# Kernel tuning notes

Measured on AMD Instinct MI355X. Metric: run time of the kernel, lower is better.

## Reference

```python
import jax, jax.numpy as jnp
import numpy as np
from jax import lax

# sRGB linear -> LMS matrix (Oklab M1)
M1 = jnp.array([[0.4122214708, 0.5363325363, 0.0514459929],
                [0.2119034982, 0.6806995451, 0.1073969566],
                [0.0883024619, 0.2817188376, 0.6299787005]], dtype=jnp.float32)
# LMS^(1/3) -> Oklab matrix (Oklab M2)
M2 = jnp.array([[0.2104542553, 0.7936177850, -0.0040720468],
                [1.9779984951, -2.4285922050, 0.4505937099],
                [0.0259040371, 0.7827717662, -0.8086757660]], dtype=jnp.float32)
_SX = jnp.array([[-1., 0., 1.], [-2., 0., 2.], [-1., 0., 1.]], dtype=jnp.float32)
_SY = jnp.array([[-1., -2., -1.], [0., 0., 0.], [1., 2., 1.]], dtype=jnp.float32)
SOBEL = jnp.stack([_SX, _SY])[:, None]  # (2,1,3,3) cross-correlation kernels

CLOSING_KERNEL = 11
CLOSING_PAD = CLOSING_KERNEL // 2
EDGE_THRESHOLD = 0.5
POST_DILATION = 2
EPS = 0.01


def _srgb_to_linear(srgb):
    srgb = jnp.clip(srgb, 0.0, 1.0)
    return jnp.where(srgb <= 0.04045, srgb / 12.92, ((srgb + 0.055) / 1.055) ** 2.4)


def _rgb_to_oklab(rgb):  # [B,3,H,W] -> [B,3,H,W]
    linear = _srgb_to_linear(rgb)
    lms = jnp.einsum('oc,bchw->bohw', M1, linear)
    lms = jnp.clip(lms, 1e-10, None) ** (1.0 / 3.0)
    return jnp.einsum('oc,bchw->bohw', M2, lms)


def _max_pool(x, k, p):  # torch max_pool2d pads with -inf implicitly
    return lax.reduce_window(x, -jnp.inf, lax.max, (1, 1, k, k), (1, 1, 1, 1),
                             [(0, 0), (0, 0), (p, p), (p, p)])


def _min_pool(x, k, p):  # -max_pool(-x): padding becomes +inf
    return lax.reduce_window(x, jnp.inf, lax.min, (1, 1, k, k), (1, 1, 1, 1),
                             [(0, 0), (0, 0), (p, p), (p, p)])


def _omni_edge(img):  # [B,C,H,W] -> [B,1,H,W]
    B, C, H, W = img.shape
    flat = img.reshape(B * C, 1, H, W)
    g = lax.conv_general_dilated(flat, SOBEL, (1, 1), [(1, 1), (1, 1)])  # [B*C,2,H,W]
    grad = (jnp.abs(g[:, 0]) + jnp.abs(g[:, 1])).reshape(B, C, H, W)
    return jnp.max(grad, axis=1, keepdims=True)


def _crevice_mask(target):
    edge_soft = jnp.clip(_omni_edge(target) / EDGE_THRESHOLD, 0.0, 1.0)
    dilated = _max_pool(edge_soft, CLOSING_KERNEL, CLOSING_PAD)
    closed = _min_pool(dilated, CLOSING_KERNEL, CLOSING_PAD)
    mask = jax.nn.relu(closed - edge_soft)
    if POST_DILATION > 0:
        dk = 2 * POST_DILATION + 1
        mask = _max_pool(mask, dk, POST_DILATION)
    return mask


def setup_inputs() -> dict:
    key = jax.random.key(0)
    k1, k2 = jax.random.split(key)
    shape = (8, 3, 1024, 1024)
    pred = jax.random.uniform(k1, shape, dtype=jnp.float32)
    target = jax.random.uniform(k2, shape, dtype=jnp.float32)
    return {"pred": pred, "target": target}


def reference(pred, target):
    crevice_mask = _crevice_mask(target)
    mask_sum = jnp.maximum(crevice_mask.sum(), 1.0)
    pred_lab = _rgb_to_oklab(pred)
    target_lab = _rgb_to_oklab(target)
    p_a, p_b = pred_lab[:, 1:2], pred_lab[:, 2:3]
    t_a, t_b = target_lab[:, 1:2], target_lab[:, 2:3]
    C_pred = jnp.sqrt(p_a ** 2 + p_b ** 2 + 1e-12)
    C_gt = jnp.sqrt(t_a ** 2 + t_b ** 2 + 1e-12)
    chroma_loss = (jnp.abs(C_pred - C_gt) * crevice_mask).sum() / mask_sum
    dot_ab = p_a * t_a + p_b * t_b
    cos_hue_diff = jnp.clip(dot_ab / (C_pred * C_gt + 1e-12), -1.0, 1.0)
    hue_loss = (jnp.clip(C_gt, EPS, None) * (1.0 - cos_hue_diff) * crevice_mask).sum() / mask_sum
    return chroma_loss + 2.0 * hue_loss
```

## Files before the change

kernel.cpp:

```cpp
#include <hip/hip_runtime.h>
#include <math.h>

#define K1_NR 16
#define SROWS 64
#define PCH   16
#define QCAP  1024


__device__ __forceinline__ float srgb_to_linear(float x) {
    x = fminf(fmaxf(x, 0.0f), 1.0f);
    return (x <= 0.04045f) ? x * (1.0f / 12.92f)
                           : powf((x + 0.055f) * (1.0f / 1.055f), 2.4f);
}

__device__ __forceinline__ void oklab_ab(float r, float g, float b,
                                         float& A, float& Bc) {
    r = srgb_to_linear(r);
    g = srgb_to_linear(g);
    b = srgb_to_linear(b);
    float l = 0.4122214708f * r + 0.5363325363f * g + 0.0514459929f * b;
    float m = 0.2119034982f * r + 0.6806995451f * g + 0.1073969566f * b;
    float s = 0.0883024619f * r + 0.2817188376f * g + 0.6299787005f * b;
    l = cbrtf(fmaxf(l, 1e-10f));
    m = cbrtf(fmaxf(m, 1e-10f));
    s = cbrtf(fmaxf(s, 1e-10f));
    A  = 1.9779984951f * l - 2.428592205f * m + 0.4505937099f * s;
    Bc = 0.0259040371f * l + 0.7827717662f * m - 0.808675766f  * s;
}

__device__ __forceinline__ void color_terms(const float* __restrict__ pred,
                                            const float* __restrict__ target,
                                            size_t off, size_t HWp, float m,
                                            float& sc, float& sh) {
    float pa, pb, ta, tb;
    oklab_ab(pred[off], pred[off + HWp], pred[off + 2 * HWp], pa, pb);
    oklab_ab(target[off], target[off + HWp], target[off + 2 * HWp], ta, tb);
    float Cp = sqrtf(pa * pa + pb * pb + 1e-12f);
    float Cg = sqrtf(ta * ta + tb * tb + 1e-12f);
    sc += fabsf(Cp - Cg) * m;
    float cosd = (pa * ta + pb * tb) / (Cp * Cg + 1e-12f);
    cosd = fminf(fmaxf(cosd, -1.0f), 1.0f);
    sh += fmaxf(Cg, 0.01f) * (1.0f - cosd) * m;
}


__global__ __launch_bounds__(256) void k1_edge(const float* __restrict__ target,
                                               float* __restrict__ edge,
                                               int H, int W) {
    int strips = H / K1_NR;
    int b   = blockIdx.x / strips;
    int ysi = blockIdx.x % strips;
    int lane = threadIdx.x & 63, q = threadIdx.x >> 6;
    int C0 = q << 8;
    int col0 = C0 + (lane << 2);
    int y0 = ysi * K1_NR;
    size_t HW = (size_t)H * W;
    const float* tb = target + (size_t)b * 3 * HW;
    float* ep = edge + (size_t)b * HW;

    int hcol = (lane == 0) ? (C0 - 1) : (C0 + 256);
    bool hen = (lane == 0 || lane == 63) && (hcol >= 0) && (hcol < W);
    int lm = (lane + 63) & 63, lp = (lane + 1) & 63;

    float4 pr[3], cu[3], nx[3];
    float hpr[3], hcu[3], hnx[3];
#pragma unroll
    for (int c = 0; c < 3; ++c) {
        const float* p = tb + (size_t)c * HW;
        if (y0 > 0) {
            pr[c]  = *(const float4*)(p + (size_t)(y0 - 1) * W + col0);
            hpr[c] = hen ? p[(size_t)(y0 - 1) * W + hcol] : 0.f;
        } else {
            pr[c] = make_float4(0.f, 0.f, 0.f, 0.f);
            hpr[c] = 0.f;
        }
        cu[c]  = *(const float4*)(p + (size_t)y0 * W + col0);
        hcu[c] = hen ? p[(size_t)y0 * W + hcol] : 0.f;
    }

#pragma unroll 2
    for (int y = y0; y < y0 + K1_NR; ++y) {
        bool okn = (y + 1 < H);
#pragma unroll
        for (int c = 0; c < 3; ++c) {
            const float* p = tb + (size_t)c * HW + (size_t)(y + 1) * W;
            nx[c]  = okn ? *(const float4*)(p + col0)
                         : make_float4(0.f, 0.f, 0.f, 0.f);
            hnx[c] = (okn && hen) ? p[hcol] : 0.f;
        }
        float4 g = make_float4(0.f, 0.f, 0.f, 0.f);
#pragma unroll
        for (int c = 0; c < 3; ++c) {
            float4 u, v;
            u.x = fmaf(2.f, cu[c].x, pr[c].x) + nx[c].x;
            u.y = fmaf(2.f, cu[c].y, pr[c].y) + nx[c].y;
            u.z = fmaf(2.f, cu[c].z, pr[c].z) + nx[c].z;
            u.w = fmaf(2.f, cu[c].w, pr[c].w) + nx[c].w;
            v.x = nx[c].x - pr[c].x;
            v.y = nx[c].y - pr[c].y;
            v.z = nx[c].z - pr[c].z;
            v.w = nx[c].w - pr[c].w;
            float hu = fmaf(2.f, hcu[c], hpr[c]) + hnx[c];
            float hv = hnx[c] - hpr[c];
            float um1 = __shfl(u.w, lm); if (lane == 0)  um1 = hu;
            float up4 = __shfl(u.x, lp); if (lane == 63) up4 = hu;
            float vm1 = __shfl(v.w, lm); if (lane == 0)  vm1 = hv;
            float vp4 = __shfl(v.x, lp); if (lane == 63) vp4 = hv;
            float4 gx, gy;
            gx.x = u.y - um1; gx.y = u.z - u.x; gx.z = u.w - u.y; gx.w = up4 - u.z;
            gy.x = fmaf(2.f, v.x, vm1) + v.y;
            gy.y = fmaf(2.f, v.y, v.x) + v.z;
            gy.z = fmaf(2.f, v.z, v.y) + v.w;
            gy.w = fmaf(2.f, v.w, v.z) + vp4;
            g.x = fmaxf(g.x, fabsf(gx.x) + fabsf(gy.x));
            g.y = fmaxf(g.y, fabsf(gx.y) + fabsf(gy.y));
            g.z = fmaxf(g.z, fabsf(gx.z) + fabsf(gy.z));
            g.w = fmaxf(g.w, fabsf(gx.w) + fabsf(gy.w));
        }
        float4 e;
        e.x = fminf(2.f * g.x, 1.f);
        e.y = fminf(2.f * g.y, 1.f);
        e.z = fminf(2.f * g.z, 1.f);
        e.w = fminf(2.f * g.w, 1.f);
        *(float4*)(ep + (size_t)y * W + col0) = e;
#pragma unroll
        for (int c = 0; c < 3; ++c) {
            pr[c] = cu[c]; cu[c] = nx[c];
            hpr[c] = hcu[c]; hcu[c] = hnx[c];
        }
    }
}


template <int R, bool ISMAX, bool SUB_EDGE>
__global__ __launch_bounds__(256) void pool_kernel(const float* __restrict__ in,
                                                   const float* __restrict__ edge,
                                                   float* __restrict__ out,
                                                   int H, int W) {
    const int OUTW = 256 - 2 * R;
    __shared__ float s_v[PCH][256];
    int cb = (W + OUTW - 1) / OUTW;
    int rs = H / SROWS;
    int blk = blockIdx.x;
    int b   = blk / (cb * rs);
    int t   = blk % (cb * rs);
    int bxi = t / rs, ysi = t % rs;
    int tid = threadIdx.x;
    int col = bxi * OUTW - R + tid;
    int cc  = min(max(col, 0), W - 1);
    size_t base = (size_t)b * H * W;
    const float* colp = in + base + cc;
    int ys = ysi * SROWS;
    bool writer = (tid >= R) && (tid < OUTW + R) && (col < W);

    for (int ph = 0; ph < SROWS / PCH; ++ph) {
        int y0 = ys + ph * PCH;
        float w[PCH + 2 * R];
#pragma unroll
        for (int k = 0; k < PCH + 2 * R; ++k) {
            int r = min(max(y0 - R + k, 0), H - 1);
            w[k] = colp[(size_t)r * W];
        }
        float v[PCH];
#pragma unroll
        for (int k = 0; k < PCH; ++k) {
            float m = w[k];
#pragma unroll
            for (int d = 1; d <= 2 * R; ++d)
                m = ISMAX ? fmaxf(m, w[k + d]) : fminf(m, w[k + d]);
            v[k] = m;
        }
        __syncthreads();
#pragma unroll
        for (int k = 0; k < PCH; ++k) s_v[k][tid] = v[k];
        __syncthreads();
        if (writer) {
#pragma unroll
            for (int k = 0; k < PCH; ++k) {
                float m = s_v[k][tid - R];
#pragma unroll
                for (int d = 1; d <= 2 * R; ++d)
                    m = ISMAX ? fmaxf(m, s_v[k][tid - R + d])
                              : fminf(m, s_v[k][tid - R + d]);
                size_t gi = base + (size_t)(y0 + k) * W + col;
                out[gi] = SUB_EDGE ? fmaxf(m - edge[gi], 0.f) : m;
            }
        }
    }
}


__global__ __launch_bounds__(256) void k4_loss(const float* __restrict__ pred,
                                               const float* __restrict__ target,
                                               const float* __restrict__ mask0,
                                               float* __restrict__ partials,
                                               int H, int W, int nb) {
    const int R = 2, OUTW = 256 - 2 * R;
    __shared__ float s_v[PCH][256];
    __shared__ int   q_pos[QCAP];
    __shared__ float q_m[QCAP];
    __shared__ int   cnt;
    __shared__ float s_red[3][4];

    int cb = (W + OUTW - 1) / OUTW;
    int rs = H / SROWS;
    int blk = blockIdx.x;
    int b   = blk / (cb * rs);
    int t   = blk % (cb * rs);
    int bxi = t / rs, ysi = t % rs;
    int tid = threadIdx.x;
    int col = bxi * OUTW - R + tid;
    int cc  = min(max(col, 0), W - 1);
    size_t HWp  = (size_t)H * W;
    size_t base = (size_t)b * HWp;
    size_t cbase = (size_t)b * 3 * HWp;
    const float* colp = mask0 + base + cc;
    int ys = ysi * SROWS;
    bool writer = (tid >= R) && (tid < OUTW + R) && (col < W);

    float sm = 0.f, sc = 0.f, sh = 0.f;

    for (int ph = 0; ph < SROWS / PCH; ++ph) {
        int y0 = ys + ph * PCH;
        float w[PCH + 2 * R];
#pragma unroll
        for (int k = 0; k < PCH + 2 * R; ++k) {
            int r = min(max(y0 - R + k, 0), H - 1);
            w[k] = colp[(size_t)r * W];
        }
        float v[PCH];
#pragma unroll
        for (int k = 0; k < PCH; ++k) {
            float m = w[k];
#pragma unroll
            for (int d = 1; d <= 2 * R; ++d) m = fmaxf(m, w[k + d]);
            v[k] = m;
        }
        __syncthreads();
#pragma unroll
        for (int k = 0; k < PCH; ++k) s_v[k][tid] = v[k];
        if (tid == 0) cnt = 0;
        __syncthreads();
        if (writer) {
#pragma unroll
            for (int k = 0; k < PCH; ++k) {
                float m = s_v[k][tid - R];
#pragma unroll
                for (int d = 1; d <= 2 * R; ++d)
                    m = fmaxf(m, s_v[k][tid - R + d]);
                sm += m;
                if (m > 0.f) {
                    int pos = atomicAdd(&cnt, 1);
                    if (pos < QCAP) {
                        q_pos[pos] = ((y0 + k) << 16) | col;
                        q_m[pos] = m;
                    } else {
                        color_terms(pred, target,
                                    cbase + (size_t)(y0 + k) * W + col,
                                    HWp, m, sc, sh);
                    }
                }
            }
        }
        __syncthreads();
        int n = min(cnt, QCAP);
        for (int i = tid; i < n; i += 256) {
            int pk = q_pos[i];
            color_terms(pred, target,
                        cbase + (size_t)(pk >> 16) * W + (pk & 0xffff),
                        HWp, q_m[i], sc, sh);
        }
    }

#pragma unroll
    for (int off = 32; off > 0; off >>= 1) {
        sm += __shfl_down(sm, off);
        sc += __shfl_down(sc, off);
        sh += __shfl_down(sh, off);
    }
    int lane = tid & 63, wav = tid >> 6;
    __syncthreads();
    if (lane == 0) { s_red[0][wav] = sm; s_red[1][wav] = sc; s_red[2][wav] = sh; }
    __syncthreads();
    if (tid == 0) {
        float tm = 0, tc = 0, th = 0;
        for (int i = 0; i < 4; ++i) {
            tm += s_red[0][i]; tc += s_red[1][i]; th += s_red[2][i];
        }
        partials[blk]          = tm;
        partials[nb + blk]     = tc;
        partials[2 * nb + blk] = th;
    }
}

__global__ void finalize_kernel(const float* __restrict__ partials, int nb,
                                float* __restrict__ out) {
    double sm = 0.0, sc = 0.0, sh = 0.0;
    for (int i = threadIdx.x; i < nb; i += blockDim.x) {
        sm += (double)partials[i];
        sc += (double)partials[nb + i];
        sh += (double)partials[2 * nb + i];
    }
    __shared__ double red[3][256];
    red[0][threadIdx.x] = sm;
    red[1][threadIdx.x] = sc;
    red[2][threadIdx.x] = sh;
    __syncthreads();
    for (int s = blockDim.x / 2; s > 0; s >>= 1) {
        if ((int)threadIdx.x < s) {
            red[0][threadIdx.x] += red[0][threadIdx.x + s];
            red[1][threadIdx.x] += red[1][threadIdx.x + s];
            red[2][threadIdx.x] += red[2][threadIdx.x + s];
        }
        __syncthreads();
    }
    if (threadIdx.x == 0) {
        double ms = fmax(red[0][0], 1.0);
        out[0] = (float)(red[1][0] / ms + 2.0 * red[2][0] / ms);
    }
}


extern "C" void kernel_launch(void* const* d_in, const int* in_sizes, int n_in,
                              void* d_out, int out_size, void* d_ws, size_t ws_size,
                              hipStream_t stream) {
    const float* pred   = (const float*)d_in[0];
    const float* target = (const float*)d_in[1];
    float* out = (float*)d_out;

    const int H = 1024, W = 1024;
    int Bn = in_sizes[0] / (3 * H * W);
    size_t plane = (size_t)Bn * H * W * sizeof(float);

    char* ws = (char*)d_ws;
    float* planeA = (float*)ws;
    float* planeB = (float*)(ws + plane);
    float* partials = (float*)(ws + 2 * plane);

    int g1 = Bn * (H / K1_NR);
    int rs = H / SROWS;
    int cbP = (W + 245) / 246;
    int cb4 = (W + 251) / 252;
    int gP = Bn * cbP * rs;
    int g4 = Bn * cb4 * rs;

    k1_edge<<<g1, 256, 0, stream>>>(target, planeA, H, W);
    pool_kernel<5, true, false><<<gP, 256, 0, stream>>>(planeA, nullptr, planeB, H, W);
    pool_kernel<5, false, true><<<gP, 256, 0, stream>>>(planeB, planeA, planeA, H, W);
    k4_loss<<<g4, 256, 0, stream>>>(pred, target, planeA, partials, H, W, g4);
    finalize_kernel<<<1, 256, 0, stream>>>(partials, g4, out);
}
```

Before: 92.91 us.

## Fuse closing min-pool and post-dilation into loss kernel; nontemporal loads in edge

The separate min-pool kernel (closing) is merged into the loss kernel. Each block now loads a 30-row dilated window plus 20 edge rows, computes the 11x11 min, subtracts the edge, then applies the 5x5 max-pool before the color terms. This removes one full-plane write and read and one kernel launch. In exchange it adds halo recomputation (242-wide output tiles, 30-row windows per 16-row chunk) and extra shared-memory passes. The edge kernel's target loads are also switched to nontemporal.

```diff
diff --git a/kernel.cpp b/kernel.cpp
--- a/kernel.cpp
+++ b/kernel.cpp
@@ -5,7 +5,15 @@
 #define SROWS 64
 #define PCH   16
 #define QCAP  1024
-
+#define OUTW34 242
+
+
+typedef float f4v __attribute__((ext_vector_type(4)));
+
+__device__ __forceinline__ float4 nt_load4(const float* p) {
+    f4v v = __builtin_nontemporal_load((const f4v*)p);
+    return make_float4(v.x, v.y, v.z, v.w);
+}
 
 __device__ __forceinline__ float srgb_to_linear(float x) {
     x = fminf(fmaxf(x, 0.0f), 1.0f);
@@ -56,7 +64,7 @@
     int y0 = ysi * K1_NR;
     size_t HW = (size_t)H * W;
     const float* tb = target + (size_t)b * 3 * HW;
-    float* ep = edge + (size_t)b * HW;
+    float* ep = edge + (size_t)b * HW + col0;
 
     int hcol = (lane == 0) ? (C0 - 1) : (C0 + 256);
     bool hen = (lane == 0 || lane == 63) && (hcol >= 0) && (hcol < W);
@@ -68,13 +76,13 @@
     for (int c = 0; c < 3; ++c) {
         const float* p = tb + (size_t)c * HW;
         if (y0 > 0) {
-            pr[c]  = *(const float4*)(p + (size_t)(y0 - 1) * W + col0);
+            pr[c]  = nt_load4(p + (size_t)(y0 - 1) * W + col0);
             hpr[c] = hen ? p[(size_t)(y0 - 1) * W + hcol] : 0.f;
         } else {
             pr[c] = make_float4(0.f, 0.f, 0.f, 0.f);
             hpr[c] = 0.f;
         }
-        cu[c]  = *(const float4*)(p + (size_t)y0 * W + col0);
+        cu[c]  = nt_load4(p + (size_t)y0 * W + col0);
         hcu[c] = hen ? p[(size_t)y0 * W + hcol] : 0.f;
     }
 
@@ -84,7 +92,7 @@
 #pragma unroll
         for (int c = 0; c < 3; ++c) {
             const float* p = tb + (size_t)c * HW + (size_t)(y + 1) * W;
-            nx[c]  = okn ? *(const float4*)(p + col0)
+            nx[c]  = okn ? nt_load4(p + col0)
                          : make_float4(0.f, 0.f, 0.f, 0.f);
             hnx[c] = (okn && hen) ? p[hcol] : 0.f;
         }
@@ -122,7 +130,7 @@
         e.y = fminf(2.f * g.y, 1.f);
         e.z = fminf(2.f * g.z, 1.f);
         e.w = fminf(2.f * g.w, 1.f);
-        *(float4*)(ep + (size_t)y * W + col0) = e;
+        *(float4*)(ep + (size_t)y * W) = e;
 #pragma unroll
         for (int c = 0; c < 3; ++c) {
             pr[c] = cu[c]; cu[c] = nx[c];
@@ -190,73 +198,105 @@
 }
 
 
-__global__ __launch_bounds__(256) void k4_loss(const float* __restrict__ pred,
-                                               const float* __restrict__ target,
-                                               const float* __restrict__ mask0,
-                                               float* __restrict__ partials,
-                                               int H, int W, int nb) {
-    const int R = 2, OUTW = 256 - 2 * R;
-    __shared__ float s_v[PCH][256];
+__global__ __launch_bounds__(256) void k34_loss(const float* __restrict__ dil,
+                                                const float* __restrict__ edge,
+                                                const float* __restrict__ pred,
+                                                const float* __restrict__ target,
+                                                float* __restrict__ partials,
+                                                int H, int W, int nb) {
+    __shared__ float s_buf[20][256];
     __shared__ int   q_pos[QCAP];
     __shared__ float q_m[QCAP];
     __shared__ int   cnt;
     __shared__ float s_red[3][4];
 
-    int cb = (W + OUTW - 1) / OUTW;
+    int cb = (W + OUTW34 - 1) / OUTW34;
     int rs = H / SROWS;
     int blk = blockIdx.x;
     int b   = blk / (cb * rs);
-    int t   = blk % (cb * rs);
-    int bxi = t / rs, ysi = t % rs;
+    int t2  = blk % (cb * rs);
+    int bxi = t2 / rs, ysi = t2 % rs;
     int tid = threadIdx.x;
-    int col = bxi * OUTW - R + tid;
+    int col = bxi * OUTW34 - 7 + tid;
     int cc  = min(max(col, 0), W - 1);
-    size_t HWp  = (size_t)H * W;
+    size_t HWp = (size_t)H * W;
     size_t base = (size_t)b * HWp;
     size_t cbase = (size_t)b * 3 * HWp;
-    const float* colp = mask0 + base + cc;
+    const float* dcol = dil  + base + cc;
+    const float* ecol = edge + base + cc;
     int ys = ysi * SROWS;
-    bool writer = (tid >= R) && (tid < OUTW + R) && (col < W);
+    bool m0ok   = (tid >= 5) && (tid < 251);
+    bool writer = (tid >= 7) && (tid < 7 + OUTW34) && (col < W);
 
     float sm = 0.f, sc = 0.f, sh = 0.f;
 
     for (int ph = 0; ph < SROWS / PCH; ++ph) {
         int y0 = ys + ph * PCH;
-        float w[PCH + 2 * R];
-#pragma unroll
-        for (int k = 0; k < PCH + 2 * R; ++k) {
-            int r = min(max(y0 - R + k, 0), H - 1);
-            w[k] = colp[(size_t)r * W];
-        }
-        float v[PCH];
-#pragma unroll
-        for (int k = 0; k < PCH; ++k) {
-            float m = w[k];
-#pragma unroll
-            for (int d = 1; d <= 2 * R; ++d) m = fmaxf(m, w[k + d]);
-            v[k] = m;
-        }
-        __syncthreads();
-#pragma unroll
-        for (int k = 0; k < PCH; ++k) s_v[k][tid] = v[k];
+        float w[30];
+#pragma unroll
+        for (int i = 0; i < 30; ++i) {
+            int r = min(max(y0 - 7 + i, 0), H - 1);
+            w[i] = dcol[(size_t)r * W];
+        }
+        float e[20];
+#pragma unroll
+        for (int i = 0; i < 20; ++i) {
+            int r = min(max(y0 - 2 + i, 0), H - 1);
+            e[i] = ecol[(size_t)r * W];
+        }
+        float cv[20];
+#pragma unroll
+        for (int k = 0; k < 20; k += 2) {
+            float M = w[k + 1];
+#pragma unroll
+            for (int d = 2; d <= 10; ++d) M = fminf(M, w[k + d]);
+            cv[k]     = fminf(M, w[k]);
+            cv[k + 1] = fminf(M, w[k + 11]);
+        }
+        __syncthreads();
+#pragma unroll
+        for (int k = 0; k < 20; ++k) s_buf[k][tid] = cv[k];
+        __syncthreads();
+        float m0[20];
+        if (m0ok) {
+#pragma unroll
+            for (int k = 0; k < 20; ++k) {
+                float m = s_buf[k][tid - 5];
+#pragma unroll
+                for (int d = 1; d <= 10; ++d) m = fminf(m, s_buf[k][tid - 5 + d]);
+                m0[k] = fmaxf(m - e[k], 0.f);
+            }
+        }
+        __syncthreads();
+        if (m0ok) {
+#pragma unroll
+            for (int k = 0; k < 20; ++k) s_buf[k][tid] = m0[k];
+        }
         if (tid == 0) cnt = 0;
         __syncthreads();
         if (writer) {
-#pragma unroll
-            for (int k = 0; k < PCH; ++k) {
-                float m = s_v[k][tid - R];
-#pragma unroll
-                for (int d = 1; d <= 2 * R; ++d)
-                    m = fmaxf(m, s_v[k][tid - R + d]);
+            float hm[20];
+#pragma unroll
+            for (int k = 0; k < 20; ++k) {
+                float m = s_buf[k][tid - 2];
+#pragma unroll
+                for (int d = 1; d <= 4; ++d) m = fmaxf(m, s_buf[k][tid - 2 + d]);
+                hm[k] = m;
+            }
+#pragma unroll
+            for (int j = 0; j < PCH; ++j) {
+                float m = hm[j];
+#pragma unroll
+                for (int d = 1; d <= 4; ++d) m = fmaxf(m, hm[j + d]);
                 sm += m;
                 if (m > 0.f) {
                     int pos = atomicAdd(&cnt, 1);
                     if (pos < QCAP) {
-                        q_pos[pos] = ((y0 + k) << 16) | col;
-                        q_m[pos] = m;
+                        q_pos[pos] = ((y0 + j) << 16) | col;
+                        q_m[pos]   = m;
                     } else {
                         color_terms(pred, target,
-                                    cbase + (size_t)(y0 + k) * W + col,
+                                    cbase + (size_t)(y0 + j) * W + col,
                                     HWp, m, sc, sh);
                     }
                 }
@@ -340,13 +380,12 @@
     int g1 = Bn * (H / K1_NR);
     int rs = H / SROWS;
     int cbP = (W + 245) / 246;
-    int cb4 = (W + 251) / 252;
-    int gP = Bn * cbP * rs;
-    int g4 = Bn * cb4 * rs;
+    int gP  = Bn * cbP * rs;
+    int cb34 = (W + OUTW34 - 1) / OUTW34;
+    int g34  = Bn * cb34 * rs;
 
     k1_edge<<<g1, 256, 0, stream>>>(target, planeA, H, W);
     pool_kernel<5, true, false><<<gP, 256, 0, stream>>>(planeA, nullptr, planeB, H, W);
-    pool_kernel<5, false, true><<<gP, 256, 0, stream>>>(planeB, planeA, planeA, H, W);
-    k4_loss<<<g4, 256, 0, stream>>>(pred, target, planeA, partials, H, W, g4);
-    finalize_kernel<<<1, 256, 0, stream>>>(partials, g4, out);
-}
+    k34_loss<<<g34, 256, 0, stream>>>(planeB, planeA, pred, target, partials, H, W, g34);
+    finalize_kernel<<<1, 256, 0, stream>>>(partials, g34, out);
+}
```

After: 137.2 us. 47.7% more time.
